# Kernel optimization log

Hardware: AMD Instinct MI355X
Metric: run time of the kernel (lower is better)

## Reference

```python
import jax, jax.numpy as jnp
import numpy as np

NEG_SLOPE = 0.01  # PyTorch LeakyReLU default


def leaky(x):
    return jnp.where(x >= 0, x, NEG_SLOPE * x)


def conv(x, w, b, stride, pad):
    # x: NCHW, w: OIHW
    y = jax.lax.conv_general_dilated(
        x, w, (stride, stride), [(pad, pad), (pad, pad)],
        dimension_numbers=("NCHW", "OIHW", "NCHW"))
    return y + b[None, :, None, None]


def conv_transpose(x, w, b, stride, pad):
    # w has PyTorch ConvTranspose2d layout (in, out, kh, kw)
    wf = jnp.flip(w, (2, 3)).transpose(1, 0, 2, 3)  # -> (out, in, kh, kw)
    k = w.shape[2]
    p = k - 1 - pad
    y = jax.lax.conv_general_dilated(
        x, wf, (1, 1), [(p, p), (p, p)], lhs_dilation=(stride, stride),
        dimension_numbers=("NCHW", "OIHW", "NCHW"))
    return y + b[None, :, None, None]


def setup_inputs() -> dict:
    key = jax.random.key(0)
    ks = jax.random.split(key, 16)
    D, K = 64, 512
    s = 0.05
    inp = {
        "x": jax.random.normal(ks[0], (64, 1, 128, 128), jnp.float32),
        # encoder
        "ew1": jax.random.normal(ks[1], (8, 1, 4, 4), jnp.float32) * s,
        "eb1": jnp.zeros((8,), jnp.float32),
        "ew2": jax.random.normal(ks[2], (16, 8, 4, 4), jnp.float32) * s,
        "eb2": jnp.zeros((16,), jnp.float32),
        "ew3": jax.random.normal(ks[3], (16, 16, 3, 3), jnp.float32) * s,
        "eb3": jnp.zeros((16,), jnp.float32),
        "ew4": jax.random.normal(ks[4], (D, 16, 1, 1), jnp.float32) * s,
        "eb4": jnp.zeros((D,), jnp.float32),
        # codebook, init uniform(-1/K, 1/K) as in the module
        "codebook": jax.random.uniform(ks[5], (K, D), jnp.float32, -1.0 / K, 1.0 / K),
        # decoder
        "dw1": jax.random.normal(ks[6], (16, D, 3, 3), jnp.float32) * s,
        "db1": jnp.zeros((16,), jnp.float32),
        "dw2": jax.random.normal(ks[7], (16, 8, 4, 4), jnp.float32) * s,  # ConvT (in,out,k,k)
        "db2": jnp.zeros((8,), jnp.float32),
        "dw3": jax.random.normal(ks[8], (8, 1, 4, 4), jnp.float32) * s,  # ConvT (in,out,k,k)
        "db3": jnp.zeros((1,), jnp.float32),
    }
    return inp


BETA = 0.25


def vq(latents_nchw, codebook):
    # latents -> NHWC
    lat = jnp.transpose(latents_nchw, (0, 2, 3, 1))
    shp = lat.shape
    D = shp[-1]
    flat = lat.reshape(-1, D)  # [M, D]
    # pairwise squared distances to codebook [M, K]
    dist = (jnp.sum(flat ** 2, axis=1, keepdims=True)
            + jnp.sum(codebook ** 2, axis=1)
            - 2.0 * flat @ codebook.T)
    inds = jnp.argmin(dist, axis=1)  # [M]
    quant = codebook[inds].reshape(shp)  # gather == one-hot @ codebook
    commitment_loss = jnp.mean((jax.lax.stop_gradient(quant) - lat) ** 2)
    embedding_loss = jnp.mean((quant - jax.lax.stop_gradient(lat)) ** 2)
    vq_loss = commitment_loss * BETA + embedding_loss
    # straight-through estimator
    quant = lat + jax.lax.stop_gradient(quant - lat)
    return jnp.transpose(quant, (0, 3, 1, 2)), vq_loss


def reference(x, ew1, eb1, ew2, eb2, ew3, eb3, ew4, eb4, codebook,
              dw1, db1, dw2, db2, dw3, db3):
    # encoder
    h = leaky(conv(x, ew1, eb1, 2, 1))
    h = leaky(conv(h, ew2, eb2, 2, 1))
    h = leaky(conv(h, ew3, eb3, 1, 1))
    h = leaky(conv(h, ew4, eb4, 1, 0))
    # vector quantization
    q, vq_loss = vq(h, codebook)
    # decoder
    d = leaky(conv(q, dw1, db1, 1, 1))
    d = leaky(conv_transpose(d, dw2, db2, 2, 1))
    d = jnp.tanh(conv_transpose(d, dw3, db3, 2, 1))
    return d, vq_loss
```

## Files before the change

kernel.cpp:

```cpp
#include <hip/hip_runtime.h>
#include <math.h>

#define DEV __device__ __forceinline__
DEV float leakyf(float v) { return v >= 0.f ? v : 0.01f * v; }
DEV int rfl(int v) { return __builtin_amdgcn_readfirstlane(v); }

#define OFF_A    0u
#define OFF_B    2097152u
#define OFF_C    3145728u
#define OFF_D1   8388608u
#define OFF_D2   9437184u
#define OFF_IDX  11534336u
#define OFF_U    11599872u
#define OFF_C2   11673600u
#define OFF_W4T  11674112u
#define OFF_DWT  11675136u
#define OFF_LOSS 11684352u

__global__ void prep_k(const float* __restrict__ ew4, const float* __restrict__ dw1,
                       const float* __restrict__ cb, float* __restrict__ ws)
{
    int b = blockIdx.x, t = threadIdx.x;
    if (b < 4) {
        int id = b * 256 + t;
        int d = id & 63, ci = id >> 6;
        ws[OFF_W4T + id] = ew4[d * 16 + ci];
    } else if (b < 6) {
        int k = (b - 4) * 256 + t;
        float s = 0.f;
        #pragma unroll
        for (int d = 0; d < 64; ++d) { float v = cb[k * 64 + d]; s = fmaf(v, v, s); }
        ws[OFF_C2 + k] = s;
    } else {
        int id = (b - 6) * 256 + t;
        if (id < 9216) {
            int co = id & 15, tap = (id >> 4) % 9, ci = id / 144;
            ws[OFF_DWT + id] = dw1[(co * 64 + ci) * 9 + tap];
        }
    }
}

__global__ void uprep_k(const float* __restrict__ dwT, const float* __restrict__ cb,
                        float* __restrict__ U)
{
    int id = blockIdx.x * 256 + threadIdx.x;
    int k = id / 144;
    int r = id - k * 144;
    float s = 0.f;
    #pragma unroll
    for (int ci = 0; ci < 64; ++ci)
        s = fmaf(cb[k * 64 + ci], dwT[ci * 144 + r], s);
    U[id] = s;
}

template<int CIN, int COUT, int COB, int K, int S, int P, int HIN, int HOUT>
__global__ __launch_bounds__(256) void convf_k(const float* __restrict__ in,
                                               const float* __restrict__ w,
                                               const float* __restrict__ b,
                                               float* __restrict__ out)
{
    constexpr int NCG = COUT / COB;
    constexpr int WSZ = CIN * K * K * COB;
    __shared__ float wl[WSZ];
    int t = threadIdx.x;
    int idx = blockIdx.x * 256 + t;
    int x  = idx % HOUT;
    int y  = (idx / HOUT) % HOUT;
    int cg = (idx / (HOUT * HOUT)) % NCG;
    int n  = idx / (HOUT * HOUT * NCG);

    for (int i = t; i < WSZ; i += 256) {
        int co = i % COB;
        int r  = i / COB;
        int kx = r % K, ky = (r / K) % K, ci = r / (K * K);
        wl[i] = w[(((cg * COB + co) * CIN + ci) * K + ky) * K + kx];
    }
    __syncthreads();

    float acc[COB];
    #pragma unroll
    for (int j = 0; j < COB; ++j) acc[j] = b[cg * COB + j];

    const float* inn = in + n * CIN * HIN * HIN;
    for (int ci = 0; ci < CIN; ++ci) {
        #pragma unroll
        for (int ky = 0; ky < K; ++ky) {
            int iy = y * S - P + ky;
            bool vy = (iy >= 0) && (iy < HIN);
            #pragma unroll
            for (int kx = 0; kx < K; ++kx) {
                int ix = x * S - P + kx;
                float v = (vy && ix >= 0 && ix < HIN) ? inn[(ci * HIN + iy) * HIN + ix] : 0.f;
                const float* wp = &wl[((ci * K + ky) * K + kx) * COB];
                if constexpr (COB % 4 == 0) {
                    #pragma unroll
                    for (int j4 = 0; j4 < COB / 4; ++j4) {
                        float4 wv = *(const float4*)(wp + j4 * 4);
                        acc[j4 * 4 + 0] = fmaf(v, wv.x, acc[j4 * 4 + 0]);
                        acc[j4 * 4 + 1] = fmaf(v, wv.y, acc[j4 * 4 + 1]);
                        acc[j4 * 4 + 2] = fmaf(v, wv.z, acc[j4 * 4 + 2]);
                        acc[j4 * 4 + 3] = fmaf(v, wv.w, acc[j4 * 4 + 3]);
                    }
                } else {
                    #pragma unroll
                    for (int j = 0; j < COB; ++j) acc[j] = fmaf(v, wp[j], acc[j]);
                }
            }
        }
    }
    #pragma unroll
    for (int j = 0; j < COB; ++j)
        out[((n * COUT + cg * COB + j) * HOUT + y) * HOUT + x] = leakyf(acc[j]);
}

template<int CIN, int COUT, int COB, int K, int S, int P, int HIN, int HOUT, int ACT>
__global__ __launch_bounds__(256) void convtf_k(const float* __restrict__ in,
                                                const float* __restrict__ w,
                                                const float* __restrict__ b,
                                                float* __restrict__ out)
{
    constexpr int NCG = COUT / COB;
    constexpr int WSZ = CIN * K * K * COB;
    constexpr int NTAP = K / S;
    __shared__ float wl[WSZ];
    int t = threadIdx.x;
    int idx = blockIdx.x * 256 + t;
    int x  = idx % HOUT;
    int y  = (idx / HOUT) % HOUT;
    int cg = (idx / (HOUT * HOUT)) % NCG;
    int n  = idx / (HOUT * HOUT * NCG);

    for (int i = t; i < WSZ; i += 256) {
        int co = i % COB;
        int r  = i / COB;
        int kx = r % K, ky = (r / K) % K, ci = r / (K * K);
        wl[i] = w[((ci * COUT + cg * COB + co) * K + ky) * K + kx];
    }
    __syncthreads();

    float acc[COB];
    #pragma unroll
    for (int j = 0; j < COB; ++j) acc[j] = b[cg * COB + j];

    int py = (y + P) % S;
    int px = (x + P) % S;
    const float* inn = in + n * CIN * HIN * HIN;
    for (int ci = 0; ci < CIN; ++ci) {
        #pragma unroll
        for (int ty = 0; ty < NTAP; ++ty) {
            int ky = py + ty * S;
            int iy = (y + P - ky) / S;
            bool vy = (ky < K) && (iy >= 0) && (iy < HIN);
            #pragma unroll
            for (int tx = 0; tx < NTAP; ++tx) {
                int kx = px + tx * S;
                int ix = (x + P - kx) / S;
                float v = (vy && kx < K && ix >= 0 && ix < HIN)
                              ? inn[(ci * HIN + iy) * HIN + ix] : 0.f;
                const float* wp = &wl[((ci * K + ky) * K + kx) * COB];
                if constexpr (COB % 4 == 0) {
                    #pragma unroll
                    for (int j4 = 0; j4 < COB / 4; ++j4) {
                        float4 wv = *(const float4*)(wp + j4 * 4);
                        acc[j4 * 4 + 0] = fmaf(v, wv.x, acc[j4 * 4 + 0]);
                        acc[j4 * 4 + 1] = fmaf(v, wv.y, acc[j4 * 4 + 1]);
                        acc[j4 * 4 + 2] = fmaf(v, wv.z, acc[j4 * 4 + 2]);
                        acc[j4 * 4 + 3] = fmaf(v, wv.w, acc[j4 * 4 + 3]);
                    }
                } else {
                    #pragma unroll
                    for (int j = 0; j < COB; ++j) acc[j] = fmaf(v, wp[j], acc[j]);
                }
            }
        }
    }
    #pragma unroll
    for (int j = 0; j < COB; ++j) {
        float r = acc[j];
        out[((n * COUT + cg * COB + j) * HOUT + y) * HOUT + x] =
            (ACT == 0) ? leakyf(r) : tanhf(r);
    }
}

__global__ __launch_bounds__(256) void vqh_k(const float* __restrict__ h3,
                                             const float* __restrict__ w4t,
                                             const float* __restrict__ eb4,
                                             const float* __restrict__ cb,
                                             const float* __restrict__ c2,
                                             int* __restrict__ idxOut,
                                             float* __restrict__ lossAcc)
{
    __shared__ float Fs[64 * 128];
    __shared__ float Cs[64 * 128];
    int t = threadIdx.x;
    int row0 = blockIdx.x << 7;
    int n = row0 >> 10;
    int pos0 = row0 & 1023;

    {
        int row = t & 127, dh = t >> 7;
        const float* hp = h3 + (n << 14) + pos0 + row;
        float h[16];
        #pragma unroll
        for (int ci = 0; ci < 16; ++ci) h[ci] = hp[ci << 10];
        #pragma unroll
        for (int q = 0; q < 8; ++q) {
            int d0 = dh * 32 + q * 4;
            float a0 = eb4[d0 + 0], a1 = eb4[d0 + 1];
            float a2 = eb4[d0 + 2], a3 = eb4[d0 + 3];
            #pragma unroll
            for (int ci = 0; ci < 16; ++ci) {
                float v = h[ci];
                const float* wp = w4t + (ci << 6) + d0;
                a0 = fmaf(v, wp[0], a0); a1 = fmaf(v, wp[1], a1);
                a2 = fmaf(v, wp[2], a2); a3 = fmaf(v, wp[3], a3);
            }
            Fs[(d0 + 0) * 128 + row] = leakyf(a0);
            Fs[(d0 + 1) * 128 + row] = leakyf(a1);
            Fs[(d0 + 2) * 128 + row] = leakyf(a2);
            Fs[(d0 + 3) * 128 + row] = leakyf(a3);
        }
    }

    int tr = t & 15, tc = t >> 4;
    float best[8]; int bk[8];
    #pragma unroll
    for (int i = 0; i < 8; ++i) { best[i] = 3.4e38f; bk[i] = 0; }

    #pragma unroll 1
    for (int p = 0; p < 4; ++p) {
        __syncthreads();
        {
            int code = t >> 1, dh = t & 1;
            const float* src = cb + (((p << 7) + code) << 6) + dh * 32;
            #pragma unroll
            for (int q = 0; q < 8; ++q) {
                float4 v = *(const float4*)(src + q * 4);
                int d0 = dh * 32 + q * 4;
                Cs[(d0 + 0) * 128 + code] = v.x;
                Cs[(d0 + 1) * 128 + code] = v.y;
                Cs[(d0 + 2) * 128 + code] = v.z;
                Cs[(d0 + 3) * 128 + code] = v.w;
            }
        }
        __syncthreads();

        float acc[8][8];
        #pragma unroll
        for (int i = 0; i < 8; ++i)
            #pragma unroll
            for (int j = 0; j < 8; ++j) acc[i][j] = 0.f;

        const float* fp0 = &Fs[tr * 4];
        const float* fp1 = &Fs[64 + tr * 4];
        const float* cp0 = &Cs[tc * 4];
        const float* cp1 = &Cs[64 + tc * 4];
        #pragma unroll 8
        for (int d = 0; d < 64; ++d) {
            float4 f0 = *(const float4*)(fp0 + d * 128);
            float4 f1 = *(const float4*)(fp1 + d * 128);
            float4 c0 = *(const float4*)(cp0 + d * 128);
            float4 c1 = *(const float4*)(cp1 + d * 128);
            float f[8] = { f0.x, f0.y, f0.z, f0.w, f1.x, f1.y, f1.z, f1.w };
            float c[8] = { c0.x, c0.y, c0.z, c0.w, c1.x, c1.y, c1.z, c1.w };
            #pragma unroll
            for (int i = 0; i < 8; ++i)
                #pragma unroll
                for (int j = 0; j < 8; ++j)
                    acc[i][j] = fmaf(f[i], c[j], acc[i][j]);
        }
        #pragma unroll
        for (int j = 0; j < 8; ++j) {
            int kk = (p << 7) + (j < 4 ? tc * 4 + j : 64 + tc * 4 + j - 4);
            float hc2 = 0.5f * c2[kk];
            #pragma unroll
            for (int i = 0; i < 8; ++i) {
                float s = hc2 - acc[i][j];
                if (s < best[i]) { best[i] = s; bk[i] = kk; }
            }
        }
    }

    __syncthreads();
    float* redS = Cs;
    int*   redI = (int*)(Cs + 2176);
    #pragma unroll
    for (int i = 0; i < 8; ++i) {
        int row = (i < 4) ? tr * 4 + i : 64 + tr * 4 + i - 4;
        redS[row * 17 + tc] = best[i];
        redI[row * 17 + tc] = bk[i];
    }
    __syncthreads();
    if (t < 128) {
        int row = t;
        float bs = redS[row * 17]; int bi = redI[row * 17];
        #pragma unroll
        for (int c = 1; c < 16; ++c) {
            float s2 = redS[row * 17 + c];
            int   i2 = redI[row * 17 + c];
            if (s2 < bs || (s2 == bs && i2 < bi)) { bs = s2; bi = i2; }
        }
        idxOut[row0 + row] = bi;
        const float* cr = cb + (bi << 6);
        float rs = 0.f;
        #pragma unroll
        for (int d = 0; d < 64; ++d) {
            float e = cr[d] - Fs[d * 128 + row];
            rs = fmaf(e, e, rs);
        }
        #pragma unroll
        for (int off = 32; off; off >>= 1) rs += __shfl_down(rs, off, 64);
        if ((t & 63) == 0) atomicAdd(lossAcc, rs);
    }
}

__global__ __launch_bounds__(256) void d1_k(const int* __restrict__ idx,
                                            const float* __restrict__ U,
                                            const float* __restrict__ db1,
                                            float* __restrict__ out)
{
    int id = blockIdx.x * 256 + threadIdx.x;
    int x = id & 31, y = (id >> 5) & 31;
    int cg = rfl((id >> 10) & 3), n = id >> 12;
    float acc[4];
    #pragma unroll
    for (int j = 0; j < 4; ++j) acc[j] = db1[cg * 4 + j];
    const float4* U4 = (const float4*)U;
    #pragma unroll
    for (int tap = 0; tap < 9; ++tap) {
        int yy = y + tap / 3 - 1, xx = x + tap % 3 - 1;
        if (yy < 0 || yy > 31 || xx < 0 || xx > 31) continue;
        int k = idx[(n << 10) + (yy << 5) + xx];
        float4 u = U4[(k * 9 + tap) * 4 + cg];
        acc[0] += u.x; acc[1] += u.y; acc[2] += u.z; acc[3] += u.w;
    }
    #pragma unroll
    for (int j = 0; j < 4; ++j)
        out[((n * 16 + cg * 4 + j) << 10) + (y << 5) + x] = leakyf(acc[j]);
}

__global__ void loss_k(const float* __restrict__ acc, float* __restrict__ out)
{
    out[0] = 1.25f * acc[0] / 4194304.0f;
}

extern "C" void kernel_launch(void* const* d_in, const int* in_sizes, int n_in,
                              void* d_out, int out_size, void* d_ws, size_t ws_size,
                              hipStream_t stream)
{
    const float* x        = (const float*)d_in[0];
    const float* ew1      = (const float*)d_in[1];
    const float* eb1      = (const float*)d_in[2];
    const float* ew2      = (const float*)d_in[3];
    const float* eb2      = (const float*)d_in[4];
    const float* ew3      = (const float*)d_in[5];
    const float* eb3      = (const float*)d_in[6];
    const float* ew4      = (const float*)d_in[7];
    const float* eb4      = (const float*)d_in[8];
    const float* codebook = (const float*)d_in[9];
    const float* dw1      = (const float*)d_in[10];
    const float* db1      = (const float*)d_in[11];
    const float* dw2      = (const float*)d_in[12];
    const float* db2      = (const float*)d_in[13];
    const float* dw3      = (const float*)d_in[14];
    const float* db3      = (const float*)d_in[15];

    float* out = (float*)d_out;
    float* ws  = (float*)d_ws;
    float* A    = ws + OFF_A;
    float* B    = ws + OFF_B;
    float* C    = ws + OFF_C;
    float* D1   = ws + OFF_D1;
    float* D2   = ws + OFF_D2;
    int*   IDX  = (int*)(ws + OFF_IDX);
    float* U    = ws + OFF_U;
    float* C2   = ws + OFF_C2;
    float* W4T  = ws + OFF_W4T;
    float* DWT  = ws + OFF_DWT;
    float* LOSS = ws + OFF_LOSS;

    hipMemsetAsync(LOSS, 0, sizeof(float), stream);
    prep_k<<<42, 256, 0, stream>>>(ew4, dw1, codebook, ws);
    uprep_k<<<288, 256, 0, stream>>>(DWT, codebook, U);

    convf_k<1, 8, 8, 4, 2, 1, 128, 64><<<1024, 256, 0, stream>>>(x, ew1, eb1, A);
    convf_k<8, 16, 4, 4, 2, 1, 64, 32><<<1024, 256, 0, stream>>>(A, ew2, eb2, B);
    convf_k<16, 16, 4, 3, 1, 1, 32, 32><<<1024, 256, 0, stream>>>(B, ew3, eb3, C);

    vqh_k<<<512, 256, 0, stream>>>(C, W4T, eb4, codebook, C2, IDX, LOSS);

    d1_k<<<1024, 256, 0, stream>>>(IDX, U, db1, D1);
    convtf_k<16, 8, 8, 4, 2, 1, 32, 64, 0><<<1024, 256, 0, stream>>>(D1, dw2, db2, D2);
    convtf_k<8, 1, 1, 4, 2, 1, 64, 128, 1><<<4096, 256, 0, stream>>>(D2, dw3, db3, out);

    loss_k<<<1, 1, 0, stream>>>(LOSS, out + 1048576);
}
```

Measured before the change: 148.9 us.

## Use zero-padded activation buffers and sub-pixel decomposition for conv layers

Activations are now stored with a one-pixel zero halo, so each conv kernel reads a contiguous window per row without bounds checks. Transposed convs are rewritten as sub-pixel (phase) decomposition, with each thread computing a 2x2 output block from a 3x3 input neighbourhood. This removes branchy index math and the wasted divisions in the transposed path. In exchange it adds two launches, a halo-zeroing kernel and an input-padding copy, plus unaligned struct-vector loads.

```diff
diff --git a/kernel.cpp b/kernel.cpp
--- a/kernel.cpp
+++ b/kernel.cpp
@@ -5,17 +5,20 @@
 DEV float leakyf(float v) { return v >= 0.f ? v : 0.01f * v; }
 DEV int rfl(int v) { return __builtin_amdgcn_readfirstlane(v); }
 
-#define OFF_A    0u
-#define OFF_B    2097152u
-#define OFF_C    3145728u
-#define OFF_D1   8388608u
-#define OFF_D2   9437184u
-#define OFF_IDX  11534336u
-#define OFF_U    11599872u
-#define OFF_C2   11673600u
-#define OFF_W4T  11674112u
-#define OFF_DWT  11675136u
-#define OFF_LOSS 11684352u
+struct F4 { float x, y, z, w; };
+
+#define OFF_XP   0u
+#define OFF_H1P  1081600u
+#define OFF_H2P  3311872u
+#define OFF_H3   4495616u
+#define OFF_D1P  5544192u
+#define OFF_D2P  6727936u
+#define OFF_IDX  8958208u
+#define OFF_U    9023744u
+#define OFF_C2   9097472u
+#define OFF_W4T  9097984u
+#define OFF_DWT  9099008u
+#define OFF_LOSS 9108224u
 
 __global__ void prep_k(const float* __restrict__ ew4, const float* __restrict__ dw1,
                        const float* __restrict__ cb, float* __restrict__ ws)
@@ -53,133 +56,156 @@
     U[id] = s;
 }
 
-template<int CIN, int COUT, int COB, int K, int S, int P, int HIN, int HOUT>
-__global__ __launch_bounds__(256) void convf_k(const float* __restrict__ in,
-                                               const float* __restrict__ w,
-                                               const float* __restrict__ b,
-                                               float* __restrict__ out)
-{
-    constexpr int NCG = COUT / COB;
-    constexpr int WSZ = CIN * K * K * COB;
-    __shared__ float wl[WSZ];
+DEV void halo_store(float* base, int plane, int r, int W, int H, long psz)
+{
+    int row, col;
+    if (r < W)          { row = 0;     col = r; }
+    else if (r < 2 * W) { row = H - 1; col = r - W; }
+    else { int r2 = r - 2 * W; row = 1 + (r2 >> 1); col = (r2 & 1) ? W - 1 : 0; }
+    base[plane * psz + row * W + col] = 0.f;
+}
+
+__global__ void halo_k(float* __restrict__ ws)
+{
+    int id = blockIdx.x * 256 + threadIdx.x;
+    if (id < 33024) {
+        halo_store(ws + OFF_XP, id / 516, id % 516, 130, 130, 16900);
+    } else if (id < 166144) {
+        int i = id - 33024;
+        halo_store(ws + OFF_H1P, i / 260, i % 260, 66, 66, 4356);
+    } else if (id < 301312) {
+        int i = id - 166144;
+        halo_store(ws + OFF_H2P, i / 132, i % 132, 34, 34, 1156);
+    } else if (id < 436480) {
+        int i = id - 301312;
+        halo_store(ws + OFF_D1P, i / 132, i % 132, 34, 34, 1156);
+    } else if (id < 569600) {
+        int i = id - 436480;
+        halo_store(ws + OFF_D2P, i / 260, i % 260, 66, 66, 4356);
+    }
+}
+
+__global__ void padx_k(const float* __restrict__ x, float* __restrict__ xp)
+{
+    int id = blockIdx.x * 256 + threadIdx.x;
+    int ix = id & 127, iy = (id >> 7) & 127, n = id >> 14;
+    xp[(n * 130 + iy + 1) * 130 + ix + 1] = x[id];
+}
+
+__global__ __launch_bounds__(256) void e1p_k(const float* __restrict__ xp,
+                                             const float* __restrict__ ew1,
+                                             const float* __restrict__ eb1,
+                                             float* __restrict__ h1p)
+{
+    __shared__ float wl[128];
     int t = threadIdx.x;
-    int idx = blockIdx.x * 256 + t;
-    int x  = idx % HOUT;
-    int y  = (idx / HOUT) % HOUT;
-    int cg = (idx / (HOUT * HOUT)) % NCG;
-    int n  = idx / (HOUT * HOUT * NCG);
-
-    for (int i = t; i < WSZ; i += 256) {
-        int co = i % COB;
-        int r  = i / COB;
-        int kx = r % K, ky = (r / K) % K, ci = r / (K * K);
-        wl[i] = w[(((cg * COB + co) * CIN + ci) * K + ky) * K + kx];
-    }
+    if (t < 128) { int co = t & 7, tap = t >> 3; wl[t] = ew1[co * 16 + tap]; }
     __syncthreads();
-
-    float acc[COB];
-    #pragma unroll
-    for (int j = 0; j < COB; ++j) acc[j] = b[cg * COB + j];
-
-    const float* inn = in + n * CIN * HIN * HIN;
-    for (int ci = 0; ci < CIN; ++ci) {
-        #pragma unroll
-        for (int ky = 0; ky < K; ++ky) {
-            int iy = y * S - P + ky;
-            bool vy = (iy >= 0) && (iy < HIN);
-            #pragma unroll
-            for (int kx = 0; kx < K; ++kx) {
-                int ix = x * S - P + kx;
-                float v = (vy && ix >= 0 && ix < HIN) ? inn[(ci * HIN + iy) * HIN + ix] : 0.f;
-                const float* wp = &wl[((ci * K + ky) * K + kx) * COB];
-                if constexpr (COB % 4 == 0) {
-                    #pragma unroll
-                    for (int j4 = 0; j4 < COB / 4; ++j4) {
-                        float4 wv = *(const float4*)(wp + j4 * 4);
-                        acc[j4 * 4 + 0] = fmaf(v, wv.x, acc[j4 * 4 + 0]);
-                        acc[j4 * 4 + 1] = fmaf(v, wv.y, acc[j4 * 4 + 1]);
-                        acc[j4 * 4 + 2] = fmaf(v, wv.z, acc[j4 * 4 + 2]);
-                        acc[j4 * 4 + 3] = fmaf(v, wv.w, acc[j4 * 4 + 3]);
-                    }
-                } else {
-                    #pragma unroll
-                    for (int j = 0; j < COB; ++j) acc[j] = fmaf(v, wp[j], acc[j]);
-                }
-            }
-        }
-    }
-    #pragma unroll
-    for (int j = 0; j < COB; ++j)
-        out[((n * COUT + cg * COB + j) * HOUT + y) * HOUT + x] = leakyf(acc[j]);
-}
-
-template<int CIN, int COUT, int COB, int K, int S, int P, int HIN, int HOUT, int ACT>
-__global__ __launch_bounds__(256) void convtf_k(const float* __restrict__ in,
-                                                const float* __restrict__ w,
-                                                const float* __restrict__ b,
-                                                float* __restrict__ out)
-{
-    constexpr int NCG = COUT / COB;
-    constexpr int WSZ = CIN * K * K * COB;
-    constexpr int NTAP = K / S;
-    __shared__ float wl[WSZ];
+    int id = blockIdx.x * 256 + t;
+    int x = id & 63, y = (id >> 6) & 63, n = id >> 12;
+    float acc[8];
+    #pragma unroll
+    for (int j = 0; j < 8; ++j) acc[j] = eb1[j];
+    const float* base = xp + (n * 130 + 2 * y) * 130 + 2 * x;
+    #pragma unroll
+    for (int ky = 0; ky < 4; ++ky) {
+        F4 v = *(const F4*)(base + ky * 130);
+        float vv[4] = { v.x, v.y, v.z, v.w };
+        #pragma unroll
+        for (int kx = 0; kx < 4; ++kx) {
+            const float* wp = &wl[(ky * 4 + kx) * 8];
+            #pragma unroll
+            for (int j = 0; j < 8; ++j) acc[j] = fmaf(vv[kx], wp[j], acc[j]);
+        }
+    }
+    #pragma unroll
+    for (int j = 0; j < 8; ++j)
+        h1p[((n * 8 + j) * 66 + y + 1) * 66 + x + 1] = leakyf(acc[j]);
+}
+
+__global__ __launch_bounds__(256) void e2p_k(const float* __restrict__ h1p,
+                                             const float* __restrict__ ew2,
+                                             const float* __restrict__ eb2,
+                                             float* __restrict__ h2p)
+{
+    __shared__ float wl[512];
     int t = threadIdx.x;
-    int idx = blockIdx.x * 256 + t;
-    int x  = idx % HOUT;
-    int y  = (idx / HOUT) % HOUT;
-    int cg = (idx / (HOUT * HOUT)) % NCG;
-    int n  = idx / (HOUT * HOUT * NCG);
-
-    for (int i = t; i < WSZ; i += 256) {
-        int co = i % COB;
-        int r  = i / COB;
-        int kx = r % K, ky = (r / K) % K, ci = r / (K * K);
-        wl[i] = w[((ci * COUT + cg * COB + co) * K + ky) * K + kx];
+    int id = blockIdx.x * 256 + t;
+    int x = id & 31, y = (id >> 5) & 31;
+    int cg = rfl((id >> 10) & 3), n = id >> 12;
+    {
+        int i = t + (t < 256 ? 0 : 0);
+        for (i = t; i < 512; i += 256) {
+            int co = i & 3, r = i >> 2;
+            int kx = r & 3, ky = (r >> 2) & 3, ci = r >> 4;
+            wl[i] = ew2[((cg * 4 + co) * 8 + ci) * 16 + ky * 4 + kx];
+        }
     }
     __syncthreads();
-
-    float acc[COB];
-    #pragma unroll
-    for (int j = 0; j < COB; ++j) acc[j] = b[cg * COB + j];
-
-    int py = (y + P) % S;
-    int px = (x + P) % S;
-    const float* inn = in + n * CIN * HIN * HIN;
-    for (int ci = 0; ci < CIN; ++ci) {
-        #pragma unroll
-        for (int ty = 0; ty < NTAP; ++ty) {
-            int ky = py + ty * S;
-            int iy = (y + P - ky) / S;
-            bool vy = (ky < K) && (iy >= 0) && (iy < HIN);
-            #pragma unroll
-            for (int tx = 0; tx < NTAP; ++tx) {
-                int kx = px + tx * S;
-                int ix = (x + P - kx) / S;
-                float v = (vy && kx < K && ix >= 0 && ix < HIN)
-                              ? inn[(ci * HIN + iy) * HIN + ix] : 0.f;
-                const float* wp = &wl[((ci * K + ky) * K + kx) * COB];
-                if constexpr (COB % 4 == 0) {
-                    #pragma unroll
-                    for (int j4 = 0; j4 < COB / 4; ++j4) {
-                        float4 wv = *(const float4*)(wp + j4 * 4);
-                        acc[j4 * 4 + 0] = fmaf(v, wv.x, acc[j4 * 4 + 0]);
-                        acc[j4 * 4 + 1] = fmaf(v, wv.y, acc[j4 * 4 + 1]);
-                        acc[j4 * 4 + 2] = fmaf(v, wv.z, acc[j4 * 4 + 2]);
-                        acc[j4 * 4 + 3] = fmaf(v, wv.w, acc[j4 * 4 + 3]);
-                    }
-                } else {
-                    #pragma unroll
-                    for (int j = 0; j < COB; ++j) acc[j] = fmaf(v, wp[j], acc[j]);
-                }
-            }
-        }
-    }
-    #pragma unroll
-    for (int j = 0; j < COB; ++j) {
-        float r = acc[j];
-        out[((n * COUT + cg * COB + j) * HOUT + y) * HOUT + x] =
-            (ACT == 0) ? leakyf(r) : tanhf(r);
-    }
+    float acc[4];
+    #pragma unroll
+    for (int j = 0; j < 4; ++j) acc[j] = eb2[cg * 4 + j];
+    #pragma unroll 1
+    for (int ci = 0; ci < 8; ++ci) {
+        const float* base = h1p + ((n * 8 + ci) * 66 + 2 * y) * 66 + 2 * x;
+        #pragma unroll
+        for (int ky = 0; ky < 4; ++ky) {
+            F4 v = *(const F4*)(base + ky * 66);
+            float vv[4] = { v.x, v.y, v.z, v.w };
+            #pragma unroll
+            for (int kx = 0; kx < 4; ++kx) {
+                const float* wp = &wl[((ci * 4 + ky) * 4 + kx) * 4];
+                acc[0] = fmaf(vv[kx], wp[0], acc[0]);
+                acc[1] = fmaf(vv[kx], wp[1], acc[1]);
+                acc[2] = fmaf(vv[kx], wp[2], acc[2]);
+                acc[3] = fmaf(vv[kx], wp[3], acc[3]);
+            }
+        }
+    }
+    #pragma unroll
+    for (int j = 0; j < 4; ++j)
+        h2p[((n * 16 + cg * 4 + j) * 34 + y + 1) * 34 + x + 1] = leakyf(acc[j]);
+}
+
+__global__ __launch_bounds__(256) void e3p_k(const float* __restrict__ h2p,
+                                             const float* __restrict__ ew3,
+                                             const float* __restrict__ eb3,
+                                             float* __restrict__ h3)
+{
+    __shared__ float wl[576];
+    int t = threadIdx.x;
+    int id = blockIdx.x * 256 + t;
+    int x = id & 31, y = (id >> 5) & 31;
+    int cg = rfl((id >> 10) & 3), n = id >> 12;
+    for (int i = t; i < 576; i += 256) {
+        int co = i & 3, r = i >> 2;
+        int kx = r % 3, ky = (r / 3) % 3, ci = r / 9;
+        wl[i] = ew3[((cg * 4 + co) * 16 + ci) * 9 + ky * 3 + kx];
+    }
+    __syncthreads();
+    float acc[4];
+    #pragma unroll
+    for (int j = 0; j < 4; ++j) acc[j] = eb3[cg * 4 + j];
+    #pragma unroll 1
+    for (int ci = 0; ci < 16; ++ci) {
+        const float* base = h2p + ((n * 16 + ci) * 34 + y) * 34 + x;
+        #pragma unroll
+        for (int ky = 0; ky < 3; ++ky) {
+            F4 v = *(const F4*)(base + ky * 34);
+            float vv[3] = { v.x, v.y, v.z };
+            #pragma unroll
+            for (int kx = 0; kx < 3; ++kx) {
+                const float* wp = &wl[((ci * 3 + ky) * 3 + kx) * 4];
+                acc[0] = fmaf(vv[kx], wp[0], acc[0]);
+                acc[1] = fmaf(vv[kx], wp[1], acc[1]);
+                acc[2] = fmaf(vv[kx], wp[2], acc[2]);
+                acc[3] = fmaf(vv[kx], wp[3], acc[3]);
+            }
+        }
+    }
+    #pragma unroll
+    for (int j = 0; j < 4; ++j)
+        h3[((n * 16 + cg * 4 + j) << 10) + (y << 5) + x] = leakyf(acc[j]);
 }
 
 __global__ __launch_bounds__(256) void vqh_k(const float* __restrict__ h3,
@@ -314,10 +340,10 @@
     }
 }
 
-__global__ __launch_bounds__(256) void d1_k(const int* __restrict__ idx,
-                                            const float* __restrict__ U,
-                                            const float* __restrict__ db1,
-                                            float* __restrict__ out)
+__global__ __launch_bounds__(256) void d1p_k(const int* __restrict__ idx,
+                                             const float* __restrict__ U,
+                                             const float* __restrict__ db1,
+                                             float* __restrict__ d1p)
 {
     int id = blockIdx.x * 256 + threadIdx.x;
     int x = id & 31, y = (id >> 5) & 31;
@@ -336,7 +362,101 @@
     }
     #pragma unroll
     for (int j = 0; j < 4; ++j)
-        out[((n * 16 + cg * 4 + j) << 10) + (y << 5) + x] = leakyf(acc[j]);
+        d1p[((n * 16 + cg * 4 + j) * 34 + y + 1) * 34 + x + 1] = leakyf(acc[j]);
+}
+
+__global__ __launch_bounds__(256) void dt2p_k(const float* __restrict__ d1p,
+                                              const float* __restrict__ dw2,
+                                              const float* __restrict__ db2,
+                                              float* __restrict__ d2p)
+{
+    __shared__ float wl[512];
+    int t = threadIdx.x;
+    int id = blockIdx.x * 256 + t;
+    int x = id & 31, y = (id >> 5) & 31;
+    int cg = rfl((id >> 10) & 3), n = id >> 12;
+    for (int i = t; i < 512; i += 256) {
+        int co = i & 1, tap = (i >> 1) & 15, ci = i >> 5;
+        wl[i] = dw2[(ci * 8 + cg * 2 + co) * 16 + tap];
+    }
+    __syncthreads();
+    float acc[2][2][2];
+    #pragma unroll
+    for (int py = 0; py < 2; ++py)
+        #pragma unroll
+        for (int px = 0; px < 2; ++px)
+            #pragma unroll
+            for (int j = 0; j < 2; ++j) acc[py][px][j] = db2[cg * 2 + j];
+    #pragma unroll 1
+    for (int ci = 0; ci < 16; ++ci) {
+        const float* base = d1p + ((n * 16 + ci) * 34 + y) * 34 + x;
+        F4 r0 = *(const F4*)(base);
+        F4 r1 = *(const F4*)(base + 34);
+        F4 r2 = *(const F4*)(base + 68);
+        float v[3][3] = { { r0.x, r0.y, r0.z },
+                          { r1.x, r1.y, r1.z },
+                          { r2.x, r2.y, r2.z } };
+        #pragma unroll
+        for (int ky = 0; ky < 4; ++ky) {
+            int py = (ky + 1) & 1;
+            int dy = (ky == 0) ? 1 : (ky == 3 ? -1 : 0);
+            #pragma unroll
+            for (int kx = 0; kx < 4; ++kx) {
+                int px = (kx + 1) & 1;
+                int dx = (kx == 0) ? 1 : (kx == 3 ? -1 : 0);
+                float vv = v[dy + 1][dx + 1];
+                const float* wp = &wl[(ci * 16 + ky * 4 + kx) * 2];
+                acc[py][px][0] = fmaf(vv, wp[0], acc[py][px][0]);
+                acc[py][px][1] = fmaf(vv, wp[1], acc[py][px][1]);
+            }
+        }
+    }
+    #pragma unroll
+    for (int py = 0; py < 2; ++py)
+        #pragma unroll
+        for (int px = 0; px < 2; ++px)
+            #pragma unroll
+            for (int j = 0; j < 2; ++j)
+                d2p[((n * 8 + cg * 2 + j) * 66 + 2 * y + py + 1) * 66 + 2 * x + px + 1] =
+                    leakyf(acc[py][px][j]);
+}
+
+__global__ __launch_bounds__(256) void dt3p_k(const float* __restrict__ d2p,
+                                              const float* __restrict__ dw3,
+                                              const float* __restrict__ db3,
+                                              float* __restrict__ out)
+{
+    int id = blockIdx.x * 256 + threadIdx.x;
+    int x = id & 63, y = (id >> 6) & 63, n = id >> 12;
+    float b = db3[0];
+    float acc[2][2] = { { b, b }, { b, b } };
+    #pragma unroll 1
+    for (int ci = 0; ci < 8; ++ci) {
+        const float* base = d2p + ((n * 8 + ci) * 66 + y) * 66 + x;
+        F4 r0 = *(const F4*)(base);
+        F4 r1 = *(const F4*)(base + 66);
+        F4 r2 = *(const F4*)(base + 132);
+        float v[3][3] = { { r0.x, r0.y, r0.z },
+                          { r1.x, r1.y, r1.z },
+                          { r2.x, r2.y, r2.z } };
+        #pragma unroll
+        for (int ky = 0; ky < 4; ++ky) {
+            int py = (ky + 1) & 1;
+            int dy = (ky == 0) ? 1 : (ky == 3 ? -1 : 0);
+            #pragma unroll
+            for (int kx = 0; kx < 4; ++kx) {
+                int px = (kx + 1) & 1;
+                int dx = (kx == 0) ? 1 : (kx == 3 ? -1 : 0);
+                acc[py][px] = fmaf(v[dy + 1][dx + 1], dw3[ci * 16 + ky * 4 + kx],
+                                   acc[py][px]);
+            }
+        }
+    }
+    #pragma unroll
+    for (int py = 0; py < 2; ++py)
+        #pragma unroll
+        for (int px = 0; px < 2; ++px)
+            out[(n << 14) + ((2 * y + py) << 7) + 2 * x + px] = tanhf(acc[py][px]);
 }
 
 __global__ void loss_k(const float* __restrict__ acc, float* __restrict__ out)
@@ -367,11 +487,12 @@
 
     float* out = (float*)d_out;
     float* ws  = (float*)d_ws;
-    float* A    = ws + OFF_A;
-    float* B    = ws + OFF_B;
-    float* C    = ws + OFF_C;
-    float* D1   = ws + OFF_D1;
-    float* D2   = ws + OFF_D2;
+    float* XP   = ws + OFF_XP;
+    float* H1P  = ws + OFF_H1P;
+    float* H2P  = ws + OFF_H2P;
+    float* H3   = ws + OFF_H3;
+    float* D1P  = ws + OFF_D1P;
+    float* D2P  = ws + OFF_D2P;
     int*   IDX  = (int*)(ws + OFF_IDX);
     float* U    = ws + OFF_U;
     float* C2   = ws + OFF_C2;
@@ -382,16 +503,18 @@
     hipMemsetAsync(LOSS, 0, sizeof(float), stream);
     prep_k<<<42, 256, 0, stream>>>(ew4, dw1, codebook, ws);
     uprep_k<<<288, 256, 0, stream>>>(DWT, codebook, U);
-
-    convf_k<1, 8, 8, 4, 2, 1, 128, 64><<<1024, 256, 0, stream>>>(x, ew1, eb1, A);
-    convf_k<8, 16, 4, 4, 2, 1, 64, 32><<<1024, 256, 0, stream>>>(A, ew2, eb2, B);
-    convf_k<16, 16, 4, 3, 1, 1, 32, 32><<<1024, 256, 0, stream>>>(B, ew3, eb3, C);
-
-    vqh_k<<<512, 256, 0, stream>>>(C, W4T, eb4, codebook, C2, IDX, LOSS);
-
-    d1_k<<<1024, 256, 0, stream>>>(IDX, U, db1, D1);
-    convtf_k<16, 8, 8, 4, 2, 1, 32, 64, 0><<<1024, 256, 0, stream>>>(D1, dw2, db2, D2);
-    convtf_k<8, 1, 1, 4, 2, 1, 64, 128, 1><<<4096, 256, 0, stream>>>(D2, dw3, db3, out);
+    halo_k<<<2225, 256, 0, stream>>>(ws);
+    padx_k<<<4096, 256, 0, stream>>>(x, XP);
+
+    e1p_k<<<1024, 256, 0, stream>>>(XP, ew1, eb1, H1P);
+    e2p_k<<<1024, 256, 0, stream>>>(H1P, ew2, eb2, H2P);
+    e3p_k<<<1024, 256, 0, stream>>>(H2P, ew3, eb3, H3);
+
+    vqh_k<<<512, 256, 0, stream>>>(H3, W4T, eb4, codebook, C2, IDX, LOSS);
+
+    d1p_k<<<1024, 256, 0, stream>>>(IDX, U, db1, D1P);
+    dt2p_k<<<1024, 256, 0, stream>>>(D1P, dw2, db2, D2P);
+    dt3p_k<<<1024, 256, 0, stream>>>(D2P, dw3, db3, out);
 
     loss_k<<<1, 1, 0, stream>>>(LOSS, out + 1048576);
 }
```

New measurement: 148.6 us. Within noise of the previous version (-0.2%).
